# Kernel tuning notes

Hardware: AMD Instinct MI355X
Metric: run time of the kernel (lower is better)

The kernel has to match this reference:

```python
import jax, jax.numpy as jnp
import numpy as np
from jax import lax

K_NEI = 64      # max_num_neighbors in radius query
NEG = -1e30     # mask value for max-aggregation


def fps(pos, n_sample):
    """Farthest point sampling per cloud. pos: [B,N,3] -> idx [B,n_sample] int32.
    Deterministic start at point 0 (PyG uses a random start)."""
    B, N, _ = pos.shape
    start = jnp.zeros((B,), jnp.int32)
    big = jnp.full((B, N), jnp.finfo(pos.dtype).max, pos.dtype)
    def body(carry, _):
        mind, last = carry
        lp = jnp.take_along_axis(pos, last[:, None, None], axis=1)  # [B,1,3]
        d = jnp.sum((pos - lp) ** 2, -1)                            # [B,N]
        mind = jnp.minimum(mind, d)
        nxt = jnp.argmax(mind, axis=1).astype(jnp.int32)
        return (mind, nxt), nxt
    (_, _), rest = lax.scan(body, (big, start), None, length=n_sample - 1)
    return jnp.concatenate([start[None], rest], 0).T  # [B, n_sample]


def radius_nn(pos_all, pos_q, r, k):
    """Up to k nearest neighbors within radius r (per cloud).
    pos_all: [B,N,3], pos_q: [B,M,3] -> idx [B,M,k] int32, valid [B,M,k] bool."""
    d2 = jnp.sum((pos_q[:, :, None, :] - pos_all[:, None, :, :]) ** 2, -1)  # [B,M,N]
    score = jnp.where(d2 <= r * r, -d2, -jnp.inf)
    vals, idx = lax.top_k(score, k)
    return idx, jnp.isfinite(vals)


def gather(feat, idx):
    """feat: [B,P,C], idx: [B,M,k] -> [B,M,k,C]"""
    B, M, k = idx.shape
    out = jnp.take_along_axis(feat, idx.reshape(B, M * k)[:, :, None], axis=1)
    return out.reshape(B, M, k, feat.shape[-1])


def mlp3(x, w1, b1, w2, b2, w3, b3):
    x = jax.nn.relu(x @ w1 + b1)
    x = jax.nn.relu(x @ w2 + b2)
    return x @ w3 + b3


def point_conv(x, pos_src, pos_dst, nidx, valid, params):
    """PyG PointConv: message = local_nn([x_j, pos_j - pos_i]), max aggregation."""
    rel = gather(pos_src, nidx) - pos_dst[:, :, None, :]          # [B,M,k,3]
    msg = rel if x is None else jnp.concatenate([gather(x, nidx), rel], -1)
    h = mlp3(msg, *params)                                        # [B,M,k,C]
    h = jnp.where(valid[..., None], h, NEG)
    out = jnp.max(h, axis=2)
    return jnp.where(valid.any(2)[..., None], out, 0.0)


def setup_inputs() -> dict:
    key = jax.random.key(0)
    shapes = {
        'sa1_w1': (3, 64), 'sa1_b1': (64,), 'sa1_w2': (64, 64), 'sa1_b2': (64,),
        'sa1_w3': (64, 128), 'sa1_b3': (128,),
        'sa2_w1': (131, 128), 'sa2_b1': (128,), 'sa2_w2': (128, 128), 'sa2_b2': (128,),
        'sa2_w3': (128, 256), 'sa2_b3': (256,),
        'g_w1': (259, 256), 'g_b1': (256,), 'g_w2': (256, 512), 'g_b2': (512,),
        'g_w3': (512, 1024), 'g_b3': (1024,),
        'l1_w': (1024, 512), 'l1_b': (512,), 'l2_w': (512, 256), 'l2_b': (256,),
        'l3_w': (256, 7), 'l3_b': (7,),
    }
    ks = jax.random.split(key, len(shapes) + 1)
    inp = {'points': jax.random.uniform(ks[0], (8, 4096, 3), jnp.float32)}
    for i, (name, shp) in enumerate(shapes.items()):
        inp[name] = jax.random.normal(ks[i + 1], shp, jnp.float32) / np.sqrt(shp[0]).astype(np.float32)
    return inp


def reference(points, sa1_w1, sa1_b1, sa1_w2, sa1_b2, sa1_w3, sa1_b3,
              sa2_w1, sa2_b1, sa2_w2, sa2_b2, sa2_w3, sa2_b3,
              g_w1, g_b1, g_w2, g_b2, g_w3, g_b3,
              l1_w, l1_b, l2_w, l2_b, l3_w, l3_b):
    B, N, _ = points.shape
    pos = points[..., :3]
    # ---- stage 1: fps ratio 0.5, radius 0.1 ----
    N1 = N // 2
    idx1 = fps(pos, N1)
    pos1 = jnp.take_along_axis(pos, idx1[..., None], axis=1)      # [B,N1,3]
    nidx1, valid1 = radius_nn(pos, pos1, 0.1, K_NEI)
    x1 = jax.nn.relu(point_conv(None, pos, pos1, nidx1, valid1,
                                (sa1_w1, sa1_b1, sa1_w2, sa1_b2, sa1_w3, sa1_b3)))
    # ---- stage 2: fps ratio 0.25, radius 0.2 ----
    N2 = N1 // 4
    idx2 = fps(pos1, N2)
    pos2 = jnp.take_along_axis(pos1, idx2[..., None], axis=1)     # [B,N2,3]
    nidx2, valid2 = radius_nn(pos1, pos2, 0.2, K_NEI)
    x2 = jax.nn.relu(point_conv(x1, pos1, pos2, nidx2, valid2,
                                (sa2_w1, sa2_b1, sa2_w2, sa2_b2, sa2_w3, sa2_b3)))
    # ---- global MLP + grouped maxpool over 128 points ----
    g = mlp3(jnp.concatenate([x2, pos2], -1), g_w1, g_b1, g_w2, g_b2, g_w3, g_b3)  # [B,N2,1024]
    g = g.reshape(-1, 128, 1024).max(axis=1)                      # [B*N2/128, 1024]
    h = jax.nn.relu(g @ l1_w + l1_b)                              # dropout = identity (eval)
    h = jax.nn.relu(h @ l2_w + l2_b)
    h = h @ l3_w + l3_b                                           # [B*N2/128, 7]
    b_out = h.reshape(B, -1, 7).mean(axis=1)                      # [B,7]
    t = b_out[:, :3]
    q = b_out[:, 3:]
    q = q / jnp.maximum(jnp.linalg.norm(q, axis=-1, keepdims=True), 1e-12)
    return jnp.concatenate([t, q], axis=-1)
```

## Files before the change

### kernel.cpp

```cpp
#include <hip/hip_runtime.h>
#include <float.h>


typedef float f32x2 __attribute__((ext_vector_type(2)));

__device__ __forceinline__ float d2_rn(float ax, float ay, float az,
                                       float bx, float by, float bz) {
  float dx = __fsub_rn(ax, bx), dy = __fsub_rn(ay, by), dz = __fsub_rn(az, bz);
  return __fadd_rn(__fadd_rn(__fmul_rn(dx, dx), __fmul_rn(dy, dy)), __fmul_rn(dz, dz));
}

template<int CTRL>
__device__ __forceinline__ unsigned long long dppmax(unsigned long long a) {
  const unsigned int lo = (unsigned int)a, hi = (unsigned int)(a >> 32);
  const unsigned int slo =
      (unsigned int)__builtin_amdgcn_update_dpp(0, (int)lo, CTRL, 0xf, 0xf, true);
  const unsigned int shi =
      (unsigned int)__builtin_amdgcn_update_dpp(0, (int)hi, CTRL, 0xf, 0xf, true);
  const unsigned long long s = ((unsigned long long)shi << 32) | slo;
  return s > a ? s : a;
}

__device__ __forceinline__ unsigned int aload(const unsigned int* p) {
  return __hip_atomic_load(p, __ATOMIC_RELAXED, __HIP_MEMORY_SCOPE_AGENT);
}
__device__ __forceinline__ void astore(unsigned int* p, unsigned int v) {
  __hip_atomic_store(p, v, __ATOMIC_RELAXED, __HIP_MEMORY_SCOPE_AGENT);
}

__device__ __forceinline__ void barrier_lgkm() {
  asm volatile("s_waitcnt lgkmcnt(0)\n\ts_barrier" ::: "memory");
}

template<int N, int NS, int T>
__device__ void fps_core(float* sx, float* sy, float* sz,
                         unsigned long long* s_red,
                         float* __restrict__ outp,
                         unsigned int* __restrict__ pub) {
#pragma clang fp contract(off)
  constexpr int P = N / T;
  constexpr int P2 = P / 2;
  constexpr int W = T / 64;
  const int t = threadIdx.x;
  __builtin_amdgcn_s_setprio(2);
  f32x2 px[P2], py[P2], pz[P2], mind[P2];
  unsigned int kc0[P2], kc1[P2];
#pragma unroll
  for (int j = 0; j < P2; ++j) {
    const int i0 = (2*j)*T + t, i1 = i0 + T;
    px[j] = f32x2{sx[i0], sx[i1]};
    py[j] = f32x2{sy[i0], sy[i1]};
    pz[j] = f32x2{sz[i0], sz[i1]};
    mind[j] = f32x2{FLT_MAX, FLT_MAX};
    kc0[j] = (unsigned int)(N - 1 - i0);
    kc1[j] = (unsigned int)(N - 1 - i1);
  }
  float lx = sx[0], ly = sy[0], lz = sz[0];
  if (t == 0) {
    astore(&pub[0], 1u);
    outp[0] = lx; outp[1] = ly; outp[2] = lz;
  }
  for (int it = 1; it < NS; ++it) {
    const f32x2 lx2 = {lx, lx}, ly2 = {ly, ly}, lz2 = {lz, lz};
    float bv0 = -1.0f, bv1 = -1.0f;
    unsigned int bk0 = 0, bk1 = 0;
#pragma unroll
    for (int j = 0; j < P2; ++j) {
      const f32x2 dx = px[j] - lx2;
      const f32x2 dy = py[j] - ly2;
      const f32x2 dz = pz[j] - lz2;
      const f32x2 s = ((dx*dx) + (dy*dy)) + (dz*dz);
      const float m0 = fminf(mind[j].x, s.x);
      const float m1 = fminf(mind[j].y, s.y);
      mind[j] = f32x2{m0, m1};
      const bool g0 = m0 > bv0;
      bv0 = g0 ? m0 : bv0; bk0 = g0 ? kc0[j] : bk0;
      const bool g1 = m1 > bv1;
      bv1 = g1 ? m1 : bv1; bk1 = g1 ? kc1[j] : bk1;
    }
    const unsigned long long k0 = ((unsigned long long)__float_as_uint(bv0) << 32) | bk0;
    const unsigned long long k1 = ((unsigned long long)__float_as_uint(bv1) << 32) | bk1;
    unsigned long long key = k0 > k1 ? k0 : k1;
    key = dppmax<0x111>(key);
    key = dppmax<0x112>(key);
    key = dppmax<0x114>(key);
    key = dppmax<0x118>(key);
    key = dppmax<0x142>(key);
    key = dppmax<0x143>(key);
    const int par = it & 1;
    if ((t & 63) == 63) s_red[par*W + (t >> 6)] = key;
    barrier_lgkm();
    unsigned long long best = s_red[par*W];
#pragma unroll
    for (int w = 1; w < W; ++w) {
      const unsigned long long o = s_red[par*W + w];
      best = o > best ? o : best;
    }
    const int idx = (N - 1) - (int)(unsigned int)(best & 0xFFFFFFFFull);
    if (t == 0) astore(&pub[it], (unsigned int)(idx + 1));
    lx = sx[idx]; ly = sy[idx]; lz = sz[idx];
    if (t == 0) {
      outp[(size_t)it*3 + 0] = lx; outp[(size_t)it*3 + 1] = ly; outp[(size_t)it*3 + 2] = lz;
    }
  }
  __builtin_amdgcn_s_setprio(0);
}

struct FpsSm { float sx[4096], sy[4096], sz[4096]; unsigned long long red[8]; };
struct SmRC1 {
  union { struct { float d2[1024]; int id[1024]; } rad; float x[64 * 64]; } u;
  float rel[64 * 4];
  float out[128];
  int nid[64];
  int qidx;
  int cnt;
};
struct SmRC2 {
  union { struct { float d2[1024]; int id[1024]; } rad; float x[64 * 128]; } u;
  float rel[64 * 4];
  float out[256];
  int nid[64];
  int qidx;
  int cnt;
};

__device__ void rc1_item(int b, int m,
                         const float* __restrict__ points,
                         const unsigned int* __restrict__ sidx1, float r2,
                         const float* __restrict__ w1, const float* __restrict__ b1,
                         const float* __restrict__ w2, const float* __restrict__ b2,
                         const float* __restrict__ w3, const float* __restrict__ b3,
                         float* __restrict__ x1, SmRC1& R) {
  const int t = threadIdx.x;
  const int q = b*2048 + m;
  if (t == 0) {
    unsigned int v;
    while ((v = aload(&sidx1[q])) == 0u) __builtin_amdgcn_s_sleep(16);
    R.qidx = (int)v - 1;
    R.cnt = 0;
  }
  __syncthreads();
  const float* pb = points + (size_t)b * 4096 * 3;
  const int qi = R.qidx;
  const float qx = pb[qi*3], qy = pb[qi*3+1], qz = pb[qi*3+2];
  for (int i = t; i < 4096; i += 256) {
    const float d2 = d2_rn(qx, qy, qz, pb[i*3], pb[i*3+1], pb[i*3+2]);
    if (d2 <= r2) {
      const int p = atomicAdd(&R.cnt, 1);
      if (p < 1024) { R.u.rad.d2[p] = d2; R.u.rad.id[p] = i; }
    }
  }
  __syncthreads();
  const int cntc = min(R.cnt, 1024);
  const int cnt = min(cntc, 64);
  float* outp = x1 + (size_t)q * 128;
  if (cnt == 0) { if (t < 128) outp[t] = 0.f; return; }
  if (cntc <= 64) {
    if (t < cntc) R.nid[t] = R.u.rad.id[t];
  } else {
    for (int c = t; c < cntc; c += 256) {
      const float dc = R.u.rad.d2[c]; const int ic = R.u.rad.id[c];
      int rank = 0;
      for (int jj = 0; jj < cntc; ++jj)
        rank += (R.u.rad.d2[jj] < dc) || (R.u.rad.d2[jj] == dc && R.u.rad.id[jj] < ic);
      if (rank < 64) R.nid[rank] = ic;
    }
  }
  __syncthreads();
  if (t < 64) {
    const int n = (t < cnt) ? R.nid[t] : 0;
    const float* p = points + ((size_t)(b << 12) + n) * 3;
    R.rel[t*4+0] = p[0] - qx; R.rel[t*4+1] = p[1] - qy; R.rel[t*4+2] = p[2] - qz;
  }
  __syncthreads();
  const int j = t & 63;
  const int g = __builtin_amdgcn_readfirstlane(t >> 6);
  float* s_x = R.u.x;
  const int sw  = j & 31;
  const int row = j * 64;
  const float rx = R.rel[j*4+0], ry = R.rel[j*4+1], rz = R.rel[j*4+2];
  f32x2 acc[8];
  { const f32x2* bv = (const f32x2*)(b1 + g*16);
#pragma unroll
    for (int c = 0; c < 8; ++c) acc[c] = bv[c]; }
#pragma unroll
  for (int kk = 0; kk < 3; ++kk) {
    const float xk = (kk == 0) ? rx : ((kk == 1) ? ry : rz);
    const f32x2 xv = {xk, xk};
    const float4* wr = (const float4*)(w1 + kk*64 + g*16);
#pragma unroll
    for (int c4 = 0; c4 < 4; ++c4) {
      const float4 w = wr[c4];
      acc[c4*2+0] += xv * f32x2{w.x, w.y};
      acc[c4*2+1] += xv * f32x2{w.z, w.w};
    }
  }
#pragma unroll
  for (int c = 0; c < 8; ++c) {
    const f32x2 v = acc[c];
    s_x[row + ((g*16 + 2*c + 0) ^ sw)] = fmaxf(v.x, 0.f);
    s_x[row + ((g*16 + 2*c + 1) ^ sw)] = fmaxf(v.y, 0.f);
  }
  __syncthreads();
  { const f32x2* bv = (const f32x2*)(b2 + g*16);
#pragma unroll
    for (int c = 0; c < 8; ++c) acc[c] = bv[c]; }
#pragma unroll 2
  for (int k = 0; k < 64; ++k) {
    const float hk = s_x[row + (k ^ sw)];
    const f32x2 hv = {hk, hk};
    const float4* wr = (const float4*)(w2 + k*64 + g*16);
#pragma unroll
    for (int c4 = 0; c4 < 4; ++c4) {
      const float4 w = wr[c4];
      acc[c4*2+0] += hv * f32x2{w.x, w.y};
      acc[c4*2+1] += hv * f32x2{w.z, w.w};
    }
  }
  __syncthreads();
#pragma unroll
  for (int c = 0; c < 8; ++c) {
    const f32x2 v = acc[c];
    s_x[row + ((g*16 + 2*c + 0) ^ sw)] = fmaxf(v.x, 0.f);
    s_x[row + ((g*16 + 2*c + 1) ^ sw)] = fmaxf(v.y, 0.f);
  }
  __syncthreads();
#pragma unroll 1
  for (int p = 0; p < 2; ++p) {
    f32x2 a[8];
    { const f32x2* bv = (const f32x2*)(b3 + g*32 + p*16);
#pragma unroll
      for (int c = 0; c < 8; ++c) a[c] = bv[c]; }
#pragma unroll 2
    for (int k = 0; k < 64; ++k) {
      const float hk = s_x[row + (k ^ sw)];
      const f32x2 hv = {hk, hk};
      const float4* wr = (const float4*)(w3 + k*128 + g*32 + p*16);
#pragma unroll
      for (int c4 = 0; c4 < 4; ++c4) {
        const float4 w = wr[c4];
        a[c4*2+0] += hv * f32x2{w.x, w.y};
        a[c4*2+1] += hv * f32x2{w.z, w.w};
      }
    }
    if (j >= cnt) {
#pragma unroll
      for (int c = 0; c < 8; ++c) a[c] = f32x2{-1e30f, -1e30f};
    }
#pragma unroll
    for (int off = 32; off > 0; off >>= 1) {
#pragma unroll
      for (int c = 0; c < 8; ++c) {
        a[c].x = fmaxf(a[c].x, __shfl_xor(a[c].x, off, 64));
        a[c].y = fmaxf(a[c].y, __shfl_xor(a[c].y, off, 64));
      }
    }
    if (j == 0) {
#pragma unroll
      for (int c = 0; c < 8; ++c) *(f32x2*)(&R.out[g*32 + p*16 + 2*c]) = a[c];
    }
  }
  __syncthreads();
  if (t < 128) outp[t] = fmaxf(R.out[t], 0.f);
}

__global__ __launch_bounds__(256, 3) void mega1_kernel(
    const float* __restrict__ points, float* __restrict__ pos1,
    float* __restrict__ pos2,
    unsigned int* __restrict__ sidx1, unsigned int* __restrict__ sidx2,
    int* __restrict__ qhead, float r2,
    const float* __restrict__ w1, const float* __restrict__ b1,
    const float* __restrict__ w2, const float* __restrict__ b2,
    const float* __restrict__ w3, const float* __restrict__ b3,
    float* __restrict__ x1) {
  __shared__ union U { FpsSm f; SmRC1 r; } sm;
  __shared__ int s_item;
  const int t = threadIdx.x;
  for (;;) {
    __syncthreads();
    if (t == 0) s_item = atomicAdd(qhead, 1);
    __syncthreads();
    const int w = s_item;
    if (w >= 16 + 8*2048) return;
    if (w < 8) {
      const float* pb = points + (size_t)w * 4096 * 3;
      for (int i = t; i < 4096; i += 256) {
        sm.f.sx[i] = pb[i*3]; sm.f.sy[i] = pb[i*3+1]; sm.f.sz[i] = pb[i*3+2];
      }
      __syncthreads();
      fps_core<4096, 2048, 256>(sm.f.sx, sm.f.sy, sm.f.sz, sm.f.red,
                                pos1 + (size_t)w*2048*3, sidx1 + w*2048);
    } else if (w < 16) {
      const int b = w - 8;
      const float* pb = points + (size_t)b * 4096 * 3;
      for (int i = t; i < 2048; i += 256) {
        unsigned int v;
        while ((v = aload(&sidx1[b*2048 + i])) == 0u) __builtin_amdgcn_s_sleep(16);
        const int idx = (int)v - 1;
        sm.f.sx[i] = pb[idx*3]; sm.f.sy[i] = pb[idx*3+1]; sm.f.sz[i] = pb[idx*3+2];
      }
      __syncthreads();
      fps_core<2048, 512, 256>(sm.f.sx, sm.f.sy, sm.f.sz, sm.f.red,
                               pos2 + (size_t)b*512*3, sidx2 + b*512);
    } else {
      const int qq = w - 16;
      rc1_item(qq & 7, qq >> 3, points, sidx1, r2, w1, b1, w2, b2, w3, b3, x1, sm.r);
    }
  }
}

__global__ __launch_bounds__(256, 4) void rc2_kernel(
    const float* __restrict__ x1, const float* __restrict__ pos1,
    const unsigned int* __restrict__ sidx2, float r2,
    const float* __restrict__ w1, const float* __restrict__ b1,
    const float* __restrict__ w2, const float* __restrict__ b2,
    const float* __restrict__ w3, const float* __restrict__ b3,
    float* __restrict__ x2) {
  __shared__ SmRC2 R;
  const int q = blockIdx.x;
  const int b = q >> 9;
  const int t = threadIdx.x;
  if (t == 0) {
    unsigned int v;
    while ((v = aload(&sidx2[q])) == 0u) __builtin_amdgcn_s_sleep(16);
    R.qidx = (int)v - 1;
    R.cnt = 0;
  }
  __syncthreads();
  const float* pb = pos1 + (size_t)b * 2048 * 3;
  const int qi = R.qidx;
  const float qx = pb[qi*3], qy = pb[qi*3+1], qz = pb[qi*3+2];
  for (int i = t; i < 2048; i += 256) {
    const float d2 = d2_rn(qx, qy, qz, pb[i*3], pb[i*3+1], pb[i*3+2]);
    if (d2 <= r2) {
      const int p = atomicAdd(&R.cnt, 1);
      if (p < 1024) { R.u.rad.d2[p] = d2; R.u.rad.id[p] = i; }
    }
  }
  __syncthreads();
  const int cntc = min(R.cnt, 1024);
  const int cnt = min(cntc, 64);
  float* outp = x2 + (size_t)q * 256;
  if (cnt == 0) { outp[t] = 0.f; return; }
  if (cntc <= 64) {
    if (t < cntc) R.nid[t] = R.u.rad.id[t];
  } else {
    for (int c = t; c < cntc; c += 256) {
      const float dc = R.u.rad.d2[c]; const int ic = R.u.rad.id[c];
      int rank = 0;
      for (int jj = 0; jj < cntc; ++jj)
        rank += (R.u.rad.d2[jj] < dc) || (R.u.rad.d2[jj] == dc && R.u.rad.id[jj] < ic);
      if (rank < 64) R.nid[rank] = ic;
    }
  }
  __syncthreads();
  if (t < 64) {
    const int n = (t < cnt) ? R.nid[t] : 0;
    const float* p = pos1 + ((size_t)(b << 11) + n) * 3;
    R.rel[t*4+0] = p[0] - qx; R.rel[t*4+1] = p[1] - qy; R.rel[t*4+2] = p[2] - qz;
  }
  __syncthreads();
  float* s_x = R.u.x;
  for (int i = t; i < 64*128; i += 256) {
    const int r = i >> 7, c = i & 127;
    const int n = ((r < cnt) ? R.nid[r] : 0);
    s_x[r*128 + (c ^ (r & 31))] = x1[((size_t)(b << 11) + n)*128 + c];
  }
  __syncthreads();
  const int j = t & 63;
  const int g = __builtin_amdgcn_readfirstlane(t >> 6);
  const int sw  = j & 31;
  const int row = j * 128;
  f32x2 acc[16];
  { const f32x2* bv = (const f32x2*)(b1 + g*32);
#pragma unroll
    for (int c = 0; c < 16; ++c) acc[c] = bv[c]; }
#pragma unroll 2
  for (int k = 0; k < 128; ++k) {
    const float xk = s_x[row + (k ^ sw)];
    const f32x2 xv = {xk, xk};
    const float4* wr = (const float4*)(w1 + k*128 + g*32);
#pragma unroll
    for (int c4 = 0; c4 < 8; ++c4) {
      const float4 w = wr[c4];
      acc[c4*2+0] += xv * f32x2{w.x, w.y};
      acc[c4*2+1] += xv * f32x2{w.z, w.w};
    }
  }
#pragma unroll
  for (int kk = 0; kk < 3; ++kk) {
    const float xk = R.rel[j*4 + kk];
    const f32x2 xv = {xk, xk};
    const float4* wr = (const float4*)(w1 + (128 + kk)*128 + g*32);
#pragma unroll
    for (int c4 = 0; c4 < 8; ++c4) {
      const float4 w = wr[c4];
      acc[c4*2+0] += xv * f32x2{w.x, w.y};
      acc[c4*2+1] += xv * f32x2{w.z, w.w};
    }
  }
  __syncthreads();
#pragma unroll
  for (int c = 0; c < 16; ++c) {
    const f32x2 v = acc[c];
    s_x[row + ((g*32 + 2*c + 0) ^ sw)] = fmaxf(v.x, 0.f);
    s_x[row + ((g*32 + 2*c + 1) ^ sw)] = fmaxf(v.y, 0.f);
  }
  __syncthreads();
  { const f32x2* bv = (const f32x2*)(b2 + g*32);
#pragma unroll
    for (int c = 0; c < 16; ++c) acc[c] = bv[c]; }
#pragma unroll 2
  for (int k = 0; k < 128; ++k) {
    const float hk = s_x[row + (k ^ sw)];
    const f32x2 hv = {hk, hk};
    const float4* wr = (const float4*)(w2 + k*128 + g*32);
#pragma unroll
    for (int c4 = 0; c4 < 8; ++c4) {
      const float4 w = wr[c4];
      acc[c4*2+0] += hv * f32x2{w.x, w.y};
      acc[c4*2+1] += hv * f32x2{w.z, w.w};
    }
  }
  __syncthreads();
#pragma unroll
  for (int c = 0; c < 16; ++c) {
    const f32x2 v = acc[c];
    s_x[row + ((g*32 + 2*c + 0) ^ sw)] = fmaxf(v.x, 0.f);
    s_x[row + ((g*32 + 2*c + 1) ^ sw)] = fmaxf(v.y, 0.f);
  }
  __syncthreads();
#pragma unroll 1
  for (int p = 0; p < 2; ++p) {
    f32x2 a[16];
    { const f32x2* bv = (const f32x2*)(b3 + g*64 + p*32);
#pragma unroll
      for (int c = 0; c < 16; ++c) a[c] = bv[c]; }
#pragma unroll 2
    for (int k = 0; k < 128; ++k) {
      const float hk = s_x[row + (k ^ sw)];
      const f32x2 hv = {hk, hk};
      const float4* wr = (const float4*)(w3 + k*256 + g*64 + p*32);
#pragma unroll
      for (int c4 = 0; c4 < 8; ++c4) {
        const float4 w = wr[c4];
        a[c4*2+0] += hv * f32x2{w.x, w.y};
        a[c4*2+1] += hv * f32x2{w.z, w.w};
      }
    }
    if (j >= cnt) {
#pragma unroll
      for (int c = 0; c < 16; ++c) a[c] = f32x2{-1e30f, -1e30f};
    }
#pragma unroll
    for (int off = 32; off > 0; off >>= 1) {
#pragma unroll
      for (int c = 0; c < 16; ++c) {
        a[c].x = fmaxf(a[c].x, __shfl_xor(a[c].x, off, 64));
        a[c].y = fmaxf(a[c].y, __shfl_xor(a[c].y, off, 64));
      }
    }
    if (j == 0) {
#pragma unroll
      for (int c = 0; c < 16; ++c) *(f32x2*)(&R.out[g*64 + p*32 + 2*c]) = a[c];
    }
  }
  __syncthreads();
  outp[t] = fmaxf(R.out[t], 0.f);
}

__global__ __launch_bounds__(256) void gmlp_kernel(
    const float* __restrict__ x2, const float* __restrict__ pos2,
    const float* __restrict__ w1, const float* __restrict__ b1,
    const float* __restrict__ w2, const float* __restrict__ b2,
    const float* __restrict__ w3, const float* __restrict__ b3,
    float* __restrict__ gpart) {
  const int blk = blockIdx.x;
  const int t = threadIdx.x;
  __shared__ float sA[260 * 18];
  __shared__ float sB[512 * 18];
  const int p0 = blk * 16;
  for (int i = t; i < 16*256; i += 256) {
    const int p = i >> 8, k = i & 255;
    sA[k*18 + p] = x2[(size_t)(p0 + p)*256 + k];
  }
  if (t < 48) { const int p = t/3, c = t%3; sA[(256+c)*18 + p] = pos2[(size_t)(p0+p)*3 + c]; }
  __syncthreads();
  f32x2 h1[8];
  { const float bb = b1[t];
#pragma unroll
    for (int p8 = 0; p8 < 8; ++p8) h1[p8] = f32x2{bb, bb}; }
#pragma unroll 2
  for (int k = 0; k < 259; ++k) {
    const float w = w1[(size_t)k*256 + t];
    const f32x2 wv = {w, w};
    const f32x2* row = (const f32x2*)(&sA[k*18]);
#pragma unroll
    for (int p8 = 0; p8 < 8; ++p8) h1[p8] += row[p8] * wv;
  }
  __syncthreads();
#pragma unroll
  for (int p8 = 0; p8 < 8; ++p8) {
    f32x2 a = h1[p8];
    a.x = fmaxf(a.x, 0.f); a.y = fmaxf(a.y, 0.f);
    *(f32x2*)(&sA[t*18 + 2*p8]) = a;
  }
  __syncthreads();
  f32x2 h2a[8], h2b[8];
  { const float ba = b2[t], bb = b2[t + 256];
#pragma unroll
    for (int p8 = 0; p8 < 8; ++p8) { h2a[p8] = f32x2{ba, ba}; h2b[p8] = f32x2{bb, bb}; } }
#pragma unroll 2
  for (int k = 0; k < 256; ++k) {
    const float wa = w2[(size_t)k*512 + t];
    const float wb = w2[(size_t)k*512 + t + 256];
    const f32x2 wav = {wa, wa}, wbv = {wb, wb};
    const f32x2* row = (const f32x2*)(&sA[k*18]);
#pragma unroll
    for (int p8 = 0; p8 < 8; ++p8) { const f32x2 x = row[p8]; h2a[p8] += x*wav; h2b[p8] += x*wbv; }
  }
  __syncthreads();
#pragma unroll
  for (int p8 = 0; p8 < 8; ++p8) {
    f32x2 a = h2a[p8], c = h2b[p8];
    a.x = fmaxf(a.x, 0.f); a.y = fmaxf(a.y, 0.f);
    c.x = fmaxf(c.x, 0.f); c.y = fmaxf(c.y, 0.f);
    *(f32x2*)(&sB[t*18 + 2*p8]) = a;
    *(f32x2*)(&sB[(t+256)*18 + 2*p8]) = c;
  }
  __syncthreads();
  f32x2 a3[4][8];
#pragma unroll
  for (int c = 0; c < 4; ++c) {
    const float bb = b3[t + c*256];
#pragma unroll
    for (int p8 = 0; p8 < 8; ++p8) a3[c][p8] = f32x2{bb, bb};
  }
#pragma unroll 2
  for (int k = 0; k < 512; ++k) {
    const f32x2* row = (const f32x2*)(&sB[k*18]);
    f32x2 xk[8];
#pragma unroll
    for (int p8 = 0; p8 < 8; ++p8) xk[p8] = row[p8];
#pragma unroll
    for (int c = 0; c < 4; ++c) {
      const float w = w3[(size_t)k*1024 + t + c*256];
      const f32x2 wv = {w, w};
#pragma unroll
      for (int p8 = 0; p8 < 8; ++p8) a3[c][p8] += xk[p8] * wv;
    }
  }
#pragma unroll
  for (int c = 0; c < 4; ++c) {
    f32x2 m2 = a3[c][0];
#pragma unroll
    for (int p8 = 1; p8 < 8; ++p8) {
      m2.x = fmaxf(m2.x, a3[c][p8].x); m2.y = fmaxf(m2.y, a3[c][p8].y);
    }
    gpart[(size_t)blk*1024 + t + c*256] = fmaxf(m2.x, m2.y);
  }
}

__global__ __launch_bounds__(256) void head_kernel(
    const float* __restrict__ gpart,
    const float* __restrict__ l1w, const float* __restrict__ l1b,
    const float* __restrict__ l2w, const float* __restrict__ l2b,
    const float* __restrict__ l3w, const float* __restrict__ l3b,
    float* __restrict__ h3) {
  const int r = blockIdx.x, t = threadIdx.x;
  __shared__ float sIn[1024];
  __shared__ float sH[512];
  __shared__ float sH2[256];
  for (int i = t; i < 1024; i += 256) {
    float v = gpart[(size_t)(r*8)*1024 + i];
#pragma unroll
    for (int rr = 1; rr < 8; ++rr) v = fmaxf(v, gpart[(size_t)(r*8 + rr)*1024 + i]);
    sIn[i] = v;
  }
  __syncthreads();
  float a0 = l1b[t], a1 = l1b[t + 256];
#pragma unroll 4
  for (int k = 0; k < 1024; ++k) {
    const float x = sIn[k];
    a0 += x * l1w[(size_t)k*512 + t];
    a1 += x * l1w[(size_t)k*512 + t + 256];
  }
  sH[t] = fmaxf(a0, 0.f); sH[t+256] = fmaxf(a1, 0.f);
  __syncthreads();
  float a = l2b[t];
#pragma unroll 4
  for (int k = 0; k < 512; ++k) a += sH[k] * l2w[(size_t)k*256 + t];
  sH2[t] = fmaxf(a, 0.f);
  __syncthreads();
  if (t < 7) {
    float acc = l3b[t];
#pragma unroll 4
    for (int k = 0; k < 256; ++k) acc += sH2[k] * l3w[(size_t)k*7 + t];
    h3[(size_t)r*7 + t] = acc;
  }
}

__global__ void final_kernel(const float* __restrict__ h3, float* __restrict__ out) {
  const int b = threadIdx.x;
  if (b >= 8) return;
  float v[7];
#pragma unroll
  for (int c = 0; c < 7; ++c) {
    const float s = ((h3[(b*4+0)*7+c] + h3[(b*4+1)*7+c]) + h3[(b*4+2)*7+c]) + h3[(b*4+3)*7+c];
    v[c] = s * 0.25f;
  }
  const float nrm = fmaxf(sqrtf(((v[3]*v[3] + v[4]*v[4]) + v[5]*v[5]) + v[6]*v[6]), 1e-12f);
  out[b*7+0] = v[0]; out[b*7+1] = v[1]; out[b*7+2] = v[2];
  out[b*7+3] = v[3]/nrm; out[b*7+4] = v[4]/nrm;
  out[b*7+5] = v[5]/nrm; out[b*7+6] = v[6]/nrm;
}

extern "C" void kernel_launch(void* const* d_in, const int* in_sizes, int n_in,
                              void* d_out, int out_size, void* d_ws, size_t ws_size,
                              hipStream_t stream) {
  const float* points = (const float*)d_in[0];
  const float* sa1_w1 = (const float*)d_in[1];
  const float* sa1_b1 = (const float*)d_in[2];
  const float* sa1_w2 = (const float*)d_in[3];
  const float* sa1_b2 = (const float*)d_in[4];
  const float* sa1_w3 = (const float*)d_in[5];
  const float* sa1_b3 = (const float*)d_in[6];
  const float* sa2_w1 = (const float*)d_in[7];
  const float* sa2_b1 = (const float*)d_in[8];
  const float* sa2_w2 = (const float*)d_in[9];
  const float* sa2_b2 = (const float*)d_in[10];
  const float* sa2_w3 = (const float*)d_in[11];
  const float* sa2_b3 = (const float*)d_in[12];
  const float* g_w1   = (const float*)d_in[13];
  const float* g_b1   = (const float*)d_in[14];
  const float* g_w2   = (const float*)d_in[15];
  const float* g_b2   = (const float*)d_in[16];
  const float* g_w3   = (const float*)d_in[17];
  const float* g_b3   = (const float*)d_in[18];
  const float* l1_w   = (const float*)d_in[19];
  const float* l1_b   = (const float*)d_in[20];
  const float* l2_w   = (const float*)d_in[21];
  const float* l2_b   = (const float*)d_in[22];
  const float* l3_w   = (const float*)d_in[23];
  const float* l3_b   = (const float*)d_in[24];

  unsigned int* u = (unsigned int*)d_ws;
  unsigned int* sidx1 = u;
  unsigned int* sidx2 = u + 16384;
  int* qhead1 = (int*)(u + 16384 + 4096);
  const size_t syncWords = 16384 + 4096 + 1;

  float* ws = (float*)d_ws + 20608;
  size_t o = 0;
  float* pos1  = ws + o; o += (size_t)8*2048*3;
  float* pos2  = ws + o; o += (size_t)8*512*3;
  float* x1    = ws + o; o += (size_t)8*2048*128;
  float* x2    = ws + o; o += (size_t)8*512*256;
  float* gpart = ws + o; o += (size_t)256*1024;
  float* h3    = ws + o; o += (size_t)32*7;

  hipMemsetAsync(d_ws, 0, syncWords * 4, stream);

  const float R2_1 = (float)(0.1 * 0.1);
  const float R2_2 = (float)(0.2 * 0.2);

  mega1_kernel<<<768, 256, 0, stream>>>(points, pos1, pos2, sidx1, sidx2, qhead1, R2_1,
                                        sa1_w1, sa1_b1, sa1_w2, sa1_b2, sa1_w3, sa1_b3, x1);
  rc2_kernel<<<8*512, 256, 0, stream>>>(x1, pos1, sidx2, R2_2,
                                        sa2_w1, sa2_b1, sa2_w2, sa2_b2, sa2_w3, sa2_b3, x2);
  gmlp_kernel<<<256, 256, 0, stream>>>(x2, pos2, g_w1, g_b1, g_w2, g_b2, g_w3, g_b3, gpart);
  head_kernel<<<32, 256, 0, stream>>>(gpart, l1_w, l1_b, l2_w, l2_b, l3_w, l3_b, h3);
  final_kernel<<<1, 64, 0, stream>>>(h3, (float*)d_out);
}
```

Before: 2.387 ms.

## Move stage-2 FPS into a persistent mega2 kernel with one block per CU

Stage-2 farthest point sampling moves out of the first persistent kernel and into a new persistent second kernel that also pulls the stage-2 radius/conv items from its own work queue. Those items spin-wait on the FPS indices as they are published. Both kernels now launch 256 blocks and pad shared memory to 84KB, which forces one block per CU. The aim is to overlap stage-2 FPS with stage-2 convolution instead of with stage-1 work, and to give the serial FPS blocks a whole CU. The cost is far less occupancy for the compute-heavy conv items, and rc2 items can stall waiting on the slow FPS chains.

```diff
diff --git a/kernel.cpp b/kernel.cpp
--- a/kernel.cpp
+++ b/kernel.cpp
@@ -106,7 +106,8 @@
   __builtin_amdgcn_s_setprio(0);
 }
 
-struct FpsSm { float sx[4096], sy[4096], sz[4096]; unsigned long long red[8]; };
+struct FpsSm1 { float sx[4096], sy[4096], sz[4096]; unsigned long long red[8]; };
+struct FpsSm2 { float sx[2048], sy[2048], sz[2048]; unsigned long long red[8]; };
 struct SmRC1 {
   union { struct { float d2[1024]; int id[1024]; } rad; float x[64 * 64]; } u;
   float rel[64 * 4];
@@ -123,6 +124,8 @@
   int qidx;
   int cnt;
 };
+union Mega1Sm { FpsSm1 f; SmRC1 r; char pad[84 * 1024]; };
+union Mega2Sm { FpsSm2 f; SmRC2 r; char pad[84 * 1024]; };
 
 __device__ void rc1_item(int b, int m,
                          const float* __restrict__ points,
@@ -264,62 +267,15 @@
   if (t < 128) outp[t] = fmaxf(R.out[t], 0.f);
 }
 
-__global__ __launch_bounds__(256, 3) void mega1_kernel(
-    const float* __restrict__ points, float* __restrict__ pos1,
-    float* __restrict__ pos2,
-    unsigned int* __restrict__ sidx1, unsigned int* __restrict__ sidx2,
-    int* __restrict__ qhead, float r2,
-    const float* __restrict__ w1, const float* __restrict__ b1,
-    const float* __restrict__ w2, const float* __restrict__ b2,
-    const float* __restrict__ w3, const float* __restrict__ b3,
-    float* __restrict__ x1) {
-  __shared__ union U { FpsSm f; SmRC1 r; } sm;
-  __shared__ int s_item;
+__device__ void rc2_item(int b, int m,
+                         const float* __restrict__ x1, const float* __restrict__ pos1,
+                         const unsigned int* __restrict__ sidx2, float r2,
+                         const float* __restrict__ w1, const float* __restrict__ b1,
+                         const float* __restrict__ w2, const float* __restrict__ b2,
+                         const float* __restrict__ w3, const float* __restrict__ b3,
+                         float* __restrict__ x2, SmRC2& R) {
   const int t = threadIdx.x;
-  for (;;) {
-    __syncthreads();
-    if (t == 0) s_item = atomicAdd(qhead, 1);
-    __syncthreads();
-    const int w = s_item;
-    if (w >= 16 + 8*2048) return;
-    if (w < 8) {
-      const float* pb = points + (size_t)w * 4096 * 3;
-      for (int i = t; i < 4096; i += 256) {
-        sm.f.sx[i] = pb[i*3]; sm.f.sy[i] = pb[i*3+1]; sm.f.sz[i] = pb[i*3+2];
-      }
-      __syncthreads();
-      fps_core<4096, 2048, 256>(sm.f.sx, sm.f.sy, sm.f.sz, sm.f.red,
-                                pos1 + (size_t)w*2048*3, sidx1 + w*2048);
-    } else if (w < 16) {
-      const int b = w - 8;
-      const float* pb = points + (size_t)b * 4096 * 3;
-      for (int i = t; i < 2048; i += 256) {
-        unsigned int v;
-        while ((v = aload(&sidx1[b*2048 + i])) == 0u) __builtin_amdgcn_s_sleep(16);
-        const int idx = (int)v - 1;
-        sm.f.sx[i] = pb[idx*3]; sm.f.sy[i] = pb[idx*3+1]; sm.f.sz[i] = pb[idx*3+2];
-      }
-      __syncthreads();
-      fps_core<2048, 512, 256>(sm.f.sx, sm.f.sy, sm.f.sz, sm.f.red,
-                               pos2 + (size_t)b*512*3, sidx2 + b*512);
-    } else {
-      const int qq = w - 16;
-      rc1_item(qq & 7, qq >> 3, points, sidx1, r2, w1, b1, w2, b2, w3, b3, x1, sm.r);
-    }
-  }
-}
-
-__global__ __launch_bounds__(256, 4) void rc2_kernel(
-    const float* __restrict__ x1, const float* __restrict__ pos1,
-    const unsigned int* __restrict__ sidx2, float r2,
-    const float* __restrict__ w1, const float* __restrict__ b1,
-    const float* __restrict__ w2, const float* __restrict__ b2,
-    const float* __restrict__ w3, const float* __restrict__ b3,
-    float* __restrict__ x2) {
-  __shared__ SmRC2 R;
-  const int q = blockIdx.x;
-  const int b = q >> 9;
-  const int t = threadIdx.x;
+  const int q = b*512 + m;
   if (t == 0) {
     unsigned int v;
     while ((v = aload(&sidx2[q])) == 0u) __builtin_amdgcn_s_sleep(16);
@@ -467,6 +423,70 @@
   }
   __syncthreads();
   outp[t] = fmaxf(R.out[t], 0.f);
+}
+
+__global__ __launch_bounds__(256, 1) void mega1_kernel(
+    const float* __restrict__ points, float* __restrict__ pos1,
+    unsigned int* __restrict__ sidx1,
+    int* __restrict__ qhead, float r2,
+    const float* __restrict__ w1, const float* __restrict__ b1,
+    const float* __restrict__ w2, const float* __restrict__ b2,
+    const float* __restrict__ w3, const float* __restrict__ b3,
+    float* __restrict__ x1) {
+  __shared__ Mega1Sm sm;
+  __shared__ int s_item;
+  const int t = threadIdx.x;
+  for (;;) {
+    __syncthreads();
+    if (t == 0) s_item = atomicAdd(qhead, 1);
+    __syncthreads();
+    const int w = s_item;
+    if (w >= 8 + 8*2048) return;
+    if (w < 8) {
+      const float* pb = points + (size_t)w * 4096 * 3;
+      for (int i = t; i < 4096; i += 256) {
+        sm.f.sx[i] = pb[i*3]; sm.f.sy[i] = pb[i*3+1]; sm.f.sz[i] = pb[i*3+2];
+      }
+      __syncthreads();
+      fps_core<4096, 2048, 256>(sm.f.sx, sm.f.sy, sm.f.sz, sm.f.red,
+                                pos1 + (size_t)w*2048*3, sidx1 + w*2048);
+    } else {
+      const int qq = w - 8;
+      rc1_item(qq & 7, qq >> 3, points, sidx1, r2, w1, b1, w2, b2, w3, b3, x1, sm.r);
+    }
+  }
+}
+
+__global__ __launch_bounds__(256, 1) void mega2_kernel(
+    const float* __restrict__ x1, const float* __restrict__ pos1,
+    float* __restrict__ pos2,
+    unsigned int* __restrict__ sidx2, int* __restrict__ qhead, float r2,
+    const float* __restrict__ w1, const float* __restrict__ b1,
+    const float* __restrict__ w2, const float* __restrict__ b2,
+    const float* __restrict__ w3, const float* __restrict__ b3,
+    float* __restrict__ x2) {
+  __shared__ Mega2Sm sm;
+  __shared__ int s_item;
+  const int t = threadIdx.x;
+  for (;;) {
+    __syncthreads();
+    if (t == 0) s_item = atomicAdd(qhead, 1);
+    __syncthreads();
+    const int w = s_item;
+    if (w >= 8 + 8*512) return;
+    if (w < 8) {
+      const float* pb = pos1 + (size_t)w * 2048 * 3;
+      for (int i = t; i < 2048; i += 256) {
+        sm.f.sx[i] = pb[i*3]; sm.f.sy[i] = pb[i*3+1]; sm.f.sz[i] = pb[i*3+2];
+      }
+      __syncthreads();
+      fps_core<2048, 512, 256>(sm.f.sx, sm.f.sy, sm.f.sz, sm.f.red,
+                               pos2 + (size_t)w*512*3, sidx2 + w*512);
+    } else {
+      const int qq = w - 8;
+      rc2_item(qq & 7, qq >> 3, x1, pos1, sidx2, r2, w1, b1, w2, b2, w3, b3, x2, sm.r);
+    }
+  }
 }
 
 __global__ __launch_bounds__(256) void gmlp_kernel(
@@ -648,7 +668,8 @@
   unsigned int* sidx1 = u;
   unsigned int* sidx2 = u + 16384;
   int* qhead1 = (int*)(u + 16384 + 4096);
-  const size_t syncWords = 16384 + 4096 + 1;
+  int* qhead2 = qhead1 + 1;
+  const size_t syncWords = 16384 + 4096 + 2;
 
   float* ws = (float*)d_ws + 20608;
   size_t o = 0;
@@ -664,9 +685,9 @@
   const float R2_1 = (float)(0.1 * 0.1);
   const float R2_2 = (float)(0.2 * 0.2);
 
-  mega1_kernel<<<768, 256, 0, stream>>>(points, pos1, pos2, sidx1, sidx2, qhead1, R2_1,
+  mega1_kernel<<<256, 256, 0, stream>>>(points, pos1, sidx1, qhead1, R2_1,
                                         sa1_w1, sa1_b1, sa1_w2, sa1_b2, sa1_w3, sa1_b3, x1);
-  rc2_kernel<<<8*512, 256, 0, stream>>>(x1, pos1, sidx2, R2_2,
+  mega2_kernel<<<256, 256, 0, stream>>>(x1, pos1, pos2, sidx2, qhead2, R2_2,
                                         sa2_w1, sa2_b1, sa2_w2, sa2_b2, sa2_w3, sa2_b3, x2);
   gmlp_kernel<<<256, 256, 0, stream>>>(x2, pos2, g_w1, g_b1, g_w2, g_b2, g_w3, g_b3, gpart);
   head_kernel<<<32, 256, 0, stream>>>(gpart, l1_w, l1_b, l2_w, l2_b, l3_w, l3_b, h3);
```

After: 3.878 ms. +62.4%, slower.
